# Kernel optimization log

Measured on AMD Instinct MI355X. Metric: run time of the kernel, lower is better.

The kernel has to match this reference:

```python
import jax, jax.numpy as jnp
import numpy as np

N = 100000   # nodes in batched graph
E = 1600000  # edges (before self-loops)
D = 128      # in_dim == hidden_dim == num_outputs
G = 64       # graphs in the batch


def setup_inputs() -> dict:
    key = jax.random.key(0)
    ks = jax.random.split(key, 8)
    s = 1.0 / np.sqrt(D)
    x = jax.random.normal(ks[0], (N, D), jnp.float32)
    src = jax.random.randint(ks[1], (E,), 0, N, dtype=jnp.int64)
    dst = jax.random.randint(ks[2], (E,), 0, N, dtype=jnp.int64)
    graph_ids = jnp.sort(jax.random.randint(ks[3], (N,), 0, G, dtype=jnp.int64))
    W0 = jax.random.normal(ks[4], (D, D), jnp.float32) * s
    W1 = jax.random.normal(ks[5], (D, D), jnp.float32) * s
    W2 = jax.random.normal(ks[6], (D, D), jnp.float32) * s
    b0 = jnp.zeros((D,), jnp.float32)
    b1 = jnp.zeros((D,), jnp.float32)
    b2 = jnp.zeros((D,), jnp.float32)
    return {"x": x, "W0": W0, "b0": b0, "W1": W1, "b1": b1,
            "W2": W2, "b2": b2, "src": src, "dst": dst, "graph_ids": graph_ids}


def reference(x, W0, b0, W1, b1, W2, b2, src, dst, graph_ids):
    n = x.shape[0]
    loops = jnp.arange(n, dtype=src.dtype)
    src_f = jnp.concatenate([src, loops])  # add self-loops once (dgl.add_self_loop)
    dst_f = jnp.concatenate([dst, loops])
    ones_e = jnp.ones(src_f.shape, x.dtype)
    deg_out = jax.ops.segment_sum(ones_e, src_f, num_segments=n)  # >=1 (self-loop)
    deg_in = jax.ops.segment_sum(ones_e, dst_f, num_segments=n)
    cs = jax.lax.rsqrt(deg_out)[:, None]  # source norm (GraphConv norm='both')
    cd = jax.lax.rsqrt(deg_in)[:, None]   # destination norm

    def gcn_layer(h, W, b):
        m = (h * cs)[src_f]                                   # [E+N, D] gather
        agg = jax.ops.segment_sum(m, dst_f, num_segments=n)   # scatter-add SpMM
        return jax.nn.relu((agg * cd) @ W + b)                # F.relu(conv(g, h))

    h = gcn_layer(x, W0, b0)
    h = gcn_layer(h, W1, b1)
    h = gcn_layer(h, W2, b2)

    # dgl.mean_nodes: per-graph mean over nodes
    sums = jax.ops.segment_sum(h, graph_ids, num_segments=G)
    cnt = jax.ops.segment_sum(jnp.ones((n, 1), h.dtype), graph_ids, num_segments=G)
    return sums / jnp.maximum(cnt, 1.0)  # [G, D] logits
```

## Files before the change

### kernel.cpp

```cpp
#include <hip/hip_runtime.h>
#include <stdint.h>

#define D 128
#define CAP 64
#define HB 128
#define CH 50000

typedef __attribute__((ext_vector_type(8))) short bf16x8;
typedef __attribute__((ext_vector_type(4))) float f32x4;
typedef __attribute__((ext_vector_type(2))) float f32x2;

__device__ inline unsigned short f2bf(float x) {
  union { float f; uint32_t u; } v; v.f = x;
  uint32_t u = v.u;
  u += 0x7fffu + ((u >> 16) & 1u);
  return (unsigned short)(u >> 16);
}
__device__ inline uint32_t packbf(float lo, float hi) {
  return (uint32_t)f2bf(lo) | ((uint32_t)f2bf(hi) << 16);
}
__device__ inline f32x2 fp8x2f(uint32_t u) {
  f32x2 r;
  asm("v_cvt_pk_f32_fp8 %0, %1" : "=v"(r) : "v"(u));
  return r;
}
__device__ inline uint32_t f2fp8x2(float a, float b) {
  uint32_t p = 0;
  asm("v_cvt_pk_fp8_f32 %0, %1, %2" : "+v"(p) : "v"(a), "v"(b));
  return p;
}

__global__ __launch_bounds__(512) void hist_kernel(
    const int* __restrict__ src, const int* __restrict__ dst,
    unsigned int* __restrict__ parts_s, unsigned int* __restrict__ parts_d,
    int E, int N,
    const float* __restrict__ W0, const float* __restrict__ W1,
    const float* __restrict__ W2, unsigned short* __restrict__ Wt,
    int* __restrict__ cnt, int G, float* __restrict__ outz, int out_total) {
  __shared__ unsigned int lbs[CH / 8];
  __shared__ unsigned int lbd[CH / 8];
  int b = blockIdx.x & (HB - 1);
  int lo = (blockIdx.x >> 7) * CH;
  for (int i = threadIdx.x; i < CH / 8; i += 512) { lbs[i] = 0; lbd[i] = 0; }
  __syncthreads();
  int per = (E + HB - 1) / HB;
  int e0 = b * per;
  int e1 = min(e0 + per, E);
  for (int e = e0 + threadIdx.x; e < e1; e += 512) {
    int rs = src[e] - lo;
    if ((unsigned)rs < CH) atomicAdd(&lbs[rs >> 3], 1u << ((rs & 7) * 4));
    int rd = dst[e] - lo;
    if ((unsigned)rd < CH) atomicAdd(&lbd[rd >> 3], 1u << ((rd & 7) * 4));
  }
  __syncthreads();
  int nu = (N + 7) / 8;
  int base = lo >> 3;
  int cu = min(CH / 8, nu - base);
  unsigned int* ps = parts_s + (size_t)b * nu + base;
  unsigned int* pd = parts_d + (size_t)b * nu + base;
  for (int i = threadIdx.x; i < cu; i += 512) { ps[i] = lbs[i]; pd[i] = lbd[i]; }

  int gs = gridDim.x * 512;
  for (int i = blockIdx.x * 512 + threadIdx.x; i < 3 * 16384; i += gs) {
    int l = i >> 14, r = i & 16383;
    int n = r >> 7, k = r & 127;
    const float* W = (l == 0) ? W0 : (l == 1) ? W1 : W2;
    Wt[i] = f2bf(W[k * 128 + n]);
  }
  for (int i = blockIdx.x * 512 + threadIdx.x; i < G; i += gs) cnt[i] = 0;
  for (int i = blockIdx.x * 512 + threadIdx.x; i < out_total; i += gs) outz[i] = 0.f;
}

__global__ __launch_bounds__(256) void scan_norm_kernel(
    const unsigned char* __restrict__ parts_s,
    const unsigned char* __restrict__ parts_d,
    unsigned char* __restrict__ offs_d,
    int* __restrict__ degd,
    float* __restrict__ cs, float* __restrict__ cd,
    const int* __restrict__ gid, int* __restrict__ cnt,
    int N, int G) {
  __shared__ int lcnt[256];
  for (int i = threadIdx.x; i < G; i += 256) lcnt[i] = 0;
  __syncthreads();

  int t = blockIdx.x * 256 + threadIdx.x;
  if (t < N) {
    int nb = N / 2;
    int half = t >> 1;
    int sh = (t & 1) * 4;
    int ds = 0, dd = 0;
    for (int bb = 0; bb < HB; bb += 16) {
      unsigned char svv[16], dvv[16];
#pragma unroll
      for (int k = 0; k < 16; k++) {
        svv[k] = parts_s[(size_t)(bb + k) * nb + half];
        dvv[k] = parts_d[(size_t)(bb + k) * nb + half];
      }
#pragma unroll
      for (int k = 0; k < 16; k++) {
        ds += (svv[k] >> sh) & 15;
        offs_d[(size_t)(bb + k) * N + t] = (unsigned char)min(dd, 255);
        dd += (dvv[k] >> sh) & 15;
      }
    }
    degd[t] = dd;
    cs[t] = rsqrtf((float)ds + 1.0f);
    cd[t] = rsqrtf((float)dd + 1.0f);
    atomicAdd(&lcnt[gid[t]], 1);
  }
  __syncthreads();
  for (int i = threadIdx.x; i < G; i += 256) {
    int c = lcnt[i];
    if (c) atomicAdd(&cnt[i], c);
  }
}

__global__ __launch_bounds__(256) void xs_kernel(
    const float* __restrict__ x, const float* __restrict__ cs,
    uint32_t* __restrict__ xs, int N) {
  int total4 = N * 32;
  int gs = gridDim.x * 256;
  for (int i = blockIdx.x * 256 + threadIdx.x; i < total4; i += gs) {
    float4 v = ((const float4*)x)[i];
    float cc = cs[i >> 5];
    uint32_t plo = f2fp8x2(v.x * cc, v.y * cc);
    uint32_t phi = f2fp8x2(v.z * cc, v.w * cc);
    xs[i] = (plo & 0xffffu) | (phi << 16);
  }
}

__global__ __launch_bounds__(512) void fill_kernel(
    const int* __restrict__ src, const int* __restrict__ dst,
    const unsigned char* __restrict__ offs_d, int* __restrict__ col, int E, int N) {
  __shared__ unsigned int lcur[CH / 8];
  int b = blockIdx.x & (HB - 1);
  int lo = (blockIdx.x >> 7) * CH;
  for (int i = threadIdx.x; i < CH / 8; i += 512) lcur[i] = 0;
  __syncthreads();
  int per = (E + HB - 1) / HB;
  int e0 = b * per;
  int e1 = min(e0 + per, E);
  const unsigned char* offb = offs_d + (size_t)b * N;
  int e = e0 + threadIdx.x;
  for (; e + 1536 < e1; e += 2048) {
    int dd4[4], ss4[4], rd4[4];
    unsigned char ob4[4];
#pragma unroll
    for (int k = 0; k < 4; k++) { dd4[k] = dst[e + k * 512]; ss4[k] = src[e + k * 512]; }
#pragma unroll
    for (int k = 0; k < 4; k++) {
      rd4[k] = dd4[k] - lo;
      ob4[k] = ((unsigned)rd4[k] < CH) ? offb[dd4[k]] : (unsigned char)0;
    }
#pragma unroll
    for (int k = 0; k < 4; k++) {
      if ((unsigned)rd4[k] < CH) {
        unsigned old = atomicAdd(&lcur[rd4[k] >> 3], 1u << ((rd4[k] & 7) * 4));
        int local = (old >> ((rd4[k] & 7) * 4)) & 0xF;
        int pos = (int)ob4[k] + local;
        if (pos < CAP) col[(size_t)dd4[k] * CAP + pos] = ss4[k];
      }
    }
  }
  for (; e < e1; e += 512) {
    int d = dst[e];
    int rd = d - lo;
    if ((unsigned)rd < CH) {
      unsigned old = atomicAdd(&lcur[rd >> 3], 1u << ((rd & 7) * 4));
      int local = (old >> ((rd & 7) * 4)) & 0xF;
      int pos = (int)offb[d] + local;
      if (pos < CAP) col[(size_t)d * CAP + pos] = src[e];
    }
  }
}

__global__ __launch_bounds__(512) void fused_layer_kernel(
    const unsigned short* __restrict__ hin, const unsigned short* __restrict__ Wt,
    const float* __restrict__ bias, const float* __restrict__ cd,
    const float* __restrict__ rowscale, const int* __restrict__ degd,
    const int* __restrict__ col, unsigned short* __restrict__ hout, int N) {
  __shared__ __align__(16) uint32_t At[16 * 68];

  int wv = threadIdx.x >> 6;
  int lane = threadIdx.x & 63;
  int m = lane & 15;
  int quad = lane >> 4;

  bf16x8 bfr[4];
#pragma unroll
  for (int c = 0; c < 4; c++)
    bfr[c] = *(const bf16x8*)(Wt + (size_t)(16 * wv + m) * 128 + c * 32 + quad * 8);

#pragma unroll
  for (int j = 0; j < 2; j++) {
    int w = __builtin_amdgcn_readfirstlane(blockIdx.x * 16 + wv * 2 + j);
    float accx = 0.f, accy = 0.f;
    if (w < N) {
      int n = min(degd[w], CAP);
      const int* cw = col + (size_t)w * CAP;
      const unsigned short* hl = hin + lane;
      f32x2 sf = fp8x2f(hl[(size_t)w * 64]);
      accx = sf.x; accy = sf.y;
      int i = 0;
      for (; i + 7 < n; i += 8) {
        int s0 = cw[i],     s1 = cw[i + 1], s2 = cw[i + 2], s3 = cw[i + 3];
        int s4 = cw[i + 4], s5 = cw[i + 5], s6 = cw[i + 6], s7 = cw[i + 7];
        uint32_t v0 = hl[(size_t)s0 * 64];
        uint32_t v1 = hl[(size_t)s1 * 64];
        uint32_t v2 = hl[(size_t)s2 * 64];
        uint32_t v3 = hl[(size_t)s3 * 64];
        uint32_t v4 = hl[(size_t)s4 * 64];
        uint32_t v5 = hl[(size_t)s5 * 64];
        uint32_t v6 = hl[(size_t)s6 * 64];
        uint32_t v7 = hl[(size_t)s7 * 64];
        f32x2 f0 = fp8x2f(v0), f1 = fp8x2f(v1), f2 = fp8x2f(v2), f3 = fp8x2f(v3);
        f32x2 f4 = fp8x2f(v4), f5 = fp8x2f(v5), f6 = fp8x2f(v6), f7 = fp8x2f(v7);
        accx += f0.x; accy += f0.y;
        accx += f1.x; accy += f1.y;
        accx += f2.x; accy += f2.y;
        accx += f3.x; accy += f3.y;
        accx += f4.x; accy += f4.y;
        accx += f5.x; accy += f5.y;
        accx += f6.x; accy += f6.y;
        accx += f7.x; accy += f7.y;
      }
      for (; i + 3 < n; i += 4) {
        int s0 = cw[i], s1 = cw[i + 1], s2 = cw[i + 2], s3 = cw[i + 3];
        uint32_t v0 = hl[(size_t)s0 * 64];
        uint32_t v1 = hl[(size_t)s1 * 64];
        uint32_t v2 = hl[(size_t)s2 * 64];
        uint32_t v3 = hl[(size_t)s3 * 64];
        f32x2 f0 = fp8x2f(v0), f1 = fp8x2f(v1), f2 = fp8x2f(v2), f3 = fp8x2f(v3);
        accx += f0.x; accy += f0.y;
        accx += f1.x; accy += f1.y;
        accx += f2.x; accy += f2.y;
        accx += f3.x; accy += f3.y;
      }
      for (; i < n; i++) {
        f32x2 f = fp8x2f(hl[(size_t)cw[i] * 64]);
        accx += f.x; accy += f.y;
      }
      float cdv = cd[w];
      accx *= cdv; accy *= cdv;
    }
    At[(wv * 2 + j) * 68 + lane] = packbf(accx, accy);
  }
  __syncthreads();

  const unsigned short* arow = (const unsigned short*)At + m * 136;
  f32x4 acc = f32x4{0.f, 0.f, 0.f, 0.f};
#pragma unroll
  for (int c = 0; c < 4; c++) {
    bf16x8 a = *(const bf16x8*)(arow + c * 32 + quad * 8);
    acc = __builtin_amdgcn_mfma_f32_16x16x32_bf16(a, bfr[c], acc, 0, 0, 0);
  }
  int colb = 16 * wv + m;
  float bv = bias[colb];
  if (rowscale) {
    unsigned char* h8 = (unsigned char*)hout;
#pragma unroll
    for (int i = 0; i < 4; i++) {
      int r = blockIdx.x * 16 + quad * 4 + i;
      if (r < N) {
        float v = acc[i] + bv;
        v = v > 0.f ? v : 0.f;
        v *= rowscale[r];
        h8[(size_t)r * D + colb] = (unsigned char)(f2fp8x2(v, v) & 0xffu);
      }
    }
  } else {
#pragma unroll
    for (int i = 0; i < 4; i++) {
      int r = blockIdx.x * 16 + quad * 4 + i;
      if (r < N) {
        float v = acc[i] + bv;
        v = v > 0.f ? v : 0.f;
        hout[(size_t)r * D + colb] = f2bf(v);
      }
    }
  }
}

__global__ void pool_kernel(const unsigned short* __restrict__ h, const int* __restrict__ gid,
                            float* __restrict__ outsum, const int* __restrict__ cnt, int N) {
  int v0 = blockIdx.x * 64;
  if (v0 >= N) return;
  int d = threadIdx.x;
  int vend = min(v0 + 64, N);
  int cur = gid[v0];
  float acc = 0.f;
  for (int v = v0; v < vend; v++) {
    int g = gid[v];
    if (g != cur) {
      float inv = 1.0f / fmaxf((float)cnt[cur], 1.0f);
      atomicAdd(&outsum[cur * D + d], acc * inv);
      acc = 0.f; cur = g;
    }
    unsigned short hv = __builtin_nontemporal_load(&h[(size_t)v * D + d]);
    union { uint32_t u; float f; } cv; cv.u = (uint32_t)hv << 16;
    acc += cv.f;
  }
  float inv = 1.0f / fmaxf((float)cnt[cur], 1.0f);
  atomicAdd(&outsum[cur * D + d], acc * inv);
}

extern "C" void kernel_launch(void* const* d_in, const int* in_sizes, int n_in,
                              void* d_out, int out_size, void* d_ws, size_t ws_size,
                              hipStream_t stream) {
  const float* x  = (const float*)d_in[0];
  const float* W0 = (const float*)d_in[1];
  const float* b0 = (const float*)d_in[2];
  const float* W1 = (const float*)d_in[3];
  const float* b1 = (const float*)d_in[4];
  const float* W2 = (const float*)d_in[5];
  const float* b2 = (const float*)d_in[6];
  const int* src  = (const int*)d_in[7];
  const int* dst  = (const int*)d_in[8];
  const int* gid  = (const int*)d_in[9];

  const int N = in_sizes[0] / D;
  const int E = in_sizes[7];
  const int G = out_size / D;
  const int nu = (N + 7) / 8;

  uint32_t* hsA = (uint32_t*)d_ws;
  uint32_t* hsB = hsA + (size_t)N * 64;
  int* col      = (int*)(hsB + (size_t)N * 64);
  int* degd     = col + (size_t)N * CAP;
  float* csb    = (float*)(degd + N);
  float* cdb    = csb + N;
  int* cnt      = (int*)(cdb + N);
  unsigned short* Wt = (unsigned short*)(cnt + G);
  unsigned int* parts_s = (unsigned int*)(Wt + 3 * 16384);
  unsigned int* parts_d = parts_s + (size_t)HB * nu;
  unsigned char* offs_d = (unsigned char*)(parts_d + (size_t)HB * nu);

  const int nch = (N + CH - 1) / CH;
  hist_kernel<<<HB * nch, 512, 0, stream>>>(src, dst, parts_s, parts_d, E, N,
                                            W0, W1, W2, Wt, cnt, G,
                                            (float*)d_out, out_size);
  scan_norm_kernel<<<(N + 255) / 256, 256, 0, stream>>>(
      (const unsigned char*)parts_s, (const unsigned char*)parts_d, offs_d,
      degd, csb, cdb, gid, cnt, N, G);
  xs_kernel<<<1024, 256, 0, stream>>>(x, csb, hsA, N);
  fill_kernel<<<HB * nch, 512, 0, stream>>>(src, dst, offs_d, col, E, N);

  const int ltiles = (N + 15) / 16;

  fused_layer_kernel<<<ltiles, 512, 0, stream>>>((const unsigned short*)hsA, Wt, b0,
                                                 cdb, csb, degd, col,
                                                 (unsigned short*)hsB, N);
  fused_layer_kernel<<<ltiles, 512, 0, stream>>>((const unsigned short*)hsB, Wt + 16384, b1,
                                                 cdb, csb, degd, col,
                                                 (unsigned short*)hsA, N);
  fused_layer_kernel<<<ltiles, 512, 0, stream>>>((const unsigned short*)hsA, Wt + 2 * 16384, b2,
                                                 cdb, nullptr, degd, col,
                                                 (unsigned short*)hsB, N);

  pool_kernel<<<(N + 63) / 64, 128, 0, stream>>>((const unsigned short*)hsB, gid,
                                                 (float*)d_out, cnt, N);
}
```

Measured before the change: 376.9 us.

## Replace histogram/scan CSR build with chunk-bucketed routing and global atomics

Replaces the 4-bit packed shared-memory histogram, per-block prefix scan and fill kernels with a two-pass bucket sort. The first pass routes edges into 8192-node chunk buckets, and the second pass scatters them into the column array using global atomic degree counters, with chunks spread across XCD-interleaved blocks. This removes the large per-partition offset tables and the repeated full passes over the edge list, so the new path streams edges once. In exchange, slot order inside each node's column list becomes nondeterministic, the code relies on global atomics and fixed bucket capacities, and it adds memset launches.

```diff
diff --git a/kernel.cpp b/kernel.cpp
--- a/kernel.cpp
+++ b/kernel.cpp
@@ -3,8 +3,10 @@
 
 #define D 128
 #define CAP 64
-#define HB 128
-#define CH 50000
+#define NCHK 16
+#define CSH 13
+#define CNODES 8192
+#define BCAP 262144
 
 typedef __attribute__((ext_vector_type(8))) short bf16x8;
 typedef __attribute__((ext_vector_type(4))) float f32x4;
@@ -30,82 +32,106 @@
   return p;
 }
 
-__global__ __launch_bounds__(512) void hist_kernel(
+__global__ __launch_bounds__(256) void route_kernel(
     const int* __restrict__ src, const int* __restrict__ dst,
-    unsigned int* __restrict__ parts_s, unsigned int* __restrict__ parts_d,
-    int E, int N,
+    uint32_t* __restrict__ bucketD, unsigned short* __restrict__ bucketS,
+    int* __restrict__ gcurD, int* __restrict__ gcurS, int E,
     const float* __restrict__ W0, const float* __restrict__ W1,
-    const float* __restrict__ W2, unsigned short* __restrict__ Wt,
-    int* __restrict__ cnt, int G, float* __restrict__ outz, int out_total) {
-  __shared__ unsigned int lbs[CH / 8];
-  __shared__ unsigned int lbd[CH / 8];
-  int b = blockIdx.x & (HB - 1);
-  int lo = (blockIdx.x >> 7) * CH;
-  for (int i = threadIdx.x; i < CH / 8; i += 512) { lbs[i] = 0; lbd[i] = 0; }
-  __syncthreads();
-  int per = (E + HB - 1) / HB;
-  int e0 = b * per;
-  int e1 = min(e0 + per, E);
-  for (int e = e0 + threadIdx.x; e < e1; e += 512) {
-    int rs = src[e] - lo;
-    if ((unsigned)rs < CH) atomicAdd(&lbs[rs >> 3], 1u << ((rs & 7) * 4));
-    int rd = dst[e] - lo;
-    if ((unsigned)rd < CH) atomicAdd(&lbd[rd >> 3], 1u << ((rd & 7) * 4));
-  }
-  __syncthreads();
-  int nu = (N + 7) / 8;
-  int base = lo >> 3;
-  int cu = min(CH / 8, nu - base);
-  unsigned int* ps = parts_s + (size_t)b * nu + base;
-  unsigned int* pd = parts_d + (size_t)b * nu + base;
-  for (int i = threadIdx.x; i < cu; i += 512) { ps[i] = lbs[i]; pd[i] = lbd[i]; }
-
-  int gs = gridDim.x * 512;
-  for (int i = blockIdx.x * 512 + threadIdx.x; i < 3 * 16384; i += gs) {
+    const float* __restrict__ W2, unsigned short* __restrict__ Wt) {
+  __shared__ int cntD[NCHK], cntS[NCHK], baseD[NCHK], baseS[NCHK];
+  int ntiles = (E + 2047) / 2048;
+  for (int tile = blockIdx.x; tile < ntiles; tile += gridDim.x) {
+    int e0 = tile * 2048;
+    int s[8], d[8];
+#pragma unroll
+    for (int k = 0; k < 8; k++) {
+      int e = e0 + k * 256 + threadIdx.x;
+      if (e < E) { s[k] = src[e]; d[k] = dst[e]; } else { s[k] = -1; d[k] = -1; }
+    }
+    if (threadIdx.x < NCHK) { cntD[threadIdx.x] = 0; cntS[threadIdx.x] = 0; }
+    __syncthreads();
+#pragma unroll
+    for (int k = 0; k < 8; k++)
+      if (d[k] >= 0) {
+        atomicAdd(&cntD[d[k] >> CSH], 1);
+        atomicAdd(&cntS[s[k] >> CSH], 1);
+      }
+    __syncthreads();
+    if (threadIdx.x < NCHK) {
+      baseD[threadIdx.x] = atomicAdd(&gcurD[threadIdx.x], cntD[threadIdx.x]);
+      baseS[threadIdx.x] = atomicAdd(&gcurS[threadIdx.x], cntS[threadIdx.x]);
+      cntD[threadIdx.x] = 0; cntS[threadIdx.x] = 0;
+    }
+    __syncthreads();
+#pragma unroll
+    for (int k = 0; k < 8; k++)
+      if (d[k] >= 0) {
+        int cD = d[k] >> CSH;
+        int slot = atomicAdd(&cntD[cD], 1);
+        bucketD[(size_t)cD * BCAP + baseD[cD] + slot] =
+            ((uint32_t)(d[k] & (CNODES - 1)) << 17) | (uint32_t)s[k];
+        int cS = s[k] >> CSH;
+        int slot2 = atomicAdd(&cntS[cS], 1);
+        bucketS[(size_t)cS * BCAP + baseS[cS] + slot2] =
+            (unsigned short)(s[k] & (CNODES - 1));
+      }
+    __syncthreads();
+  }
+  int gs = gridDim.x * 256;
+  for (int i = blockIdx.x * 256 + threadIdx.x; i < 3 * 16384; i += gs) {
     int l = i >> 14, r = i & 16383;
     int n = r >> 7, k = r & 127;
     const float* W = (l == 0) ? W0 : (l == 1) ? W1 : W2;
     Wt[i] = f2bf(W[k * 128 + n]);
   }
-  for (int i = blockIdx.x * 512 + threadIdx.x; i < G; i += gs) cnt[i] = 0;
-  for (int i = blockIdx.x * 512 + threadIdx.x; i < out_total; i += gs) outz[i] = 0.f;
-}
-
-__global__ __launch_bounds__(256) void scan_norm_kernel(
-    const unsigned char* __restrict__ parts_s,
-    const unsigned char* __restrict__ parts_d,
-    unsigned char* __restrict__ offs_d,
-    int* __restrict__ degd,
+}
+
+__global__ __launch_bounds__(256) void scatter_kernel(
+    const uint32_t* __restrict__ bucketD, const unsigned short* __restrict__ bucketS,
+    const int* __restrict__ gcurD, const int* __restrict__ gcurS,
+    int* __restrict__ col, int* __restrict__ degd, int* __restrict__ degs,
+    int nchk) {
+  int xcd = blockIdx.x & 7;
+  int slot = blockIdx.x >> 3;
+  int two = (xcd + 8 < nchk) ? 1 : 0;
+  int c, sub, nsub;
+  if (two) {
+    if (slot < 16) { c = xcd; sub = slot; nsub = 16; }
+    else           { c = xcd + 8; sub = slot - 16; nsub = 16; }
+  } else { c = xcd; sub = slot; nsub = 32; }
+  if (c >= nchk) return;
+  int base = c * CNODES;
+  int nE = gcurD[c];
+  int lo = (int)((long long)nE * sub / nsub);
+  int hi = (int)((long long)nE * (sub + 1) / nsub);
+  const uint32_t* bd = bucketD + (size_t)c * BCAP;
+  for (int i = lo + threadIdx.x; i < hi; i += 256) {
+    uint32_t p = bd[i];
+    int dg = base + (int)(p >> 17);
+    int s = (int)(p & 0x1FFFFu);
+    int pos = atomicAdd(&degd[dg], 1);
+    if (pos < CAP) col[(size_t)dg * CAP + pos] = s;
+  }
+  int nS = gcurS[c];
+  lo = (int)((long long)nS * sub / nsub);
+  hi = (int)((long long)nS * (sub + 1) / nsub);
+  const unsigned short* bs = bucketS + (size_t)c * BCAP;
+  for (int i = lo + threadIdx.x; i < hi; i += 256) {
+    atomicAdd(&degs[base + bs[i]], 1);
+  }
+}
+
+__global__ __launch_bounds__(256) void norm_kernel(
+    const int* __restrict__ degs, const int* __restrict__ degd,
     float* __restrict__ cs, float* __restrict__ cd,
-    const int* __restrict__ gid, int* __restrict__ cnt,
-    int N, int G) {
+    const int* __restrict__ gid, int* __restrict__ cnt, int N, int G) {
   __shared__ int lcnt[256];
   for (int i = threadIdx.x; i < G; i += 256) lcnt[i] = 0;
   __syncthreads();
-
   int t = blockIdx.x * 256 + threadIdx.x;
   if (t < N) {
-    int nb = N / 2;
-    int half = t >> 1;
-    int sh = (t & 1) * 4;
-    int ds = 0, dd = 0;
-    for (int bb = 0; bb < HB; bb += 16) {
-      unsigned char svv[16], dvv[16];
-#pragma unroll
-      for (int k = 0; k < 16; k++) {
-        svv[k] = parts_s[(size_t)(bb + k) * nb + half];
-        dvv[k] = parts_d[(size_t)(bb + k) * nb + half];
-      }
-#pragma unroll
-      for (int k = 0; k < 16; k++) {
-        ds += (svv[k] >> sh) & 15;
-        offs_d[(size_t)(bb + k) * N + t] = (unsigned char)min(dd, 255);
-        dd += (dvv[k] >> sh) & 15;
-      }
-    }
-    degd[t] = dd;
-    cs[t] = rsqrtf((float)ds + 1.0f);
-    cd[t] = rsqrtf((float)dd + 1.0f);
+    cs[t] = rsqrtf((float)degs[t] + 1.0f);
+    cd[t] = rsqrtf((float)degd[t] + 1.0f);
     atomicAdd(&lcnt[gid[t]], 1);
   }
   __syncthreads();
@@ -126,51 +152,6 @@
     uint32_t plo = f2fp8x2(v.x * cc, v.y * cc);
     uint32_t phi = f2fp8x2(v.z * cc, v.w * cc);
     xs[i] = (plo & 0xffffu) | (phi << 16);
-  }
-}
-
-__global__ __launch_bounds__(512) void fill_kernel(
-    const int* __restrict__ src, const int* __restrict__ dst,
-    const unsigned char* __restrict__ offs_d, int* __restrict__ col, int E, int N) {
-  __shared__ unsigned int lcur[CH / 8];
-  int b = blockIdx.x & (HB - 1);
-  int lo = (blockIdx.x >> 7) * CH;
-  for (int i = threadIdx.x; i < CH / 8; i += 512) lcur[i] = 0;
-  __syncthreads();
-  int per = (E + HB - 1) / HB;
-  int e0 = b * per;
-  int e1 = min(e0 + per, E);
-  const unsigned char* offb = offs_d + (size_t)b * N;
-  int e = e0 + threadIdx.x;
-  for (; e + 1536 < e1; e += 2048) {
-    int dd4[4], ss4[4], rd4[4];
-    unsigned char ob4[4];
-#pragma unroll
-    for (int k = 0; k < 4; k++) { dd4[k] = dst[e + k * 512]; ss4[k] = src[e + k * 512]; }
-#pragma unroll
-    for (int k = 0; k < 4; k++) {
-      rd4[k] = dd4[k] - lo;
-      ob4[k] = ((unsigned)rd4[k] < CH) ? offb[dd4[k]] : (unsigned char)0;
-    }
-#pragma unroll
-    for (int k = 0; k < 4; k++) {
-      if ((unsigned)rd4[k] < CH) {
-        unsigned old = atomicAdd(&lcur[rd4[k] >> 3], 1u << ((rd4[k] & 7) * 4));
-        int local = (old >> ((rd4[k] & 7) * 4)) & 0xF;
-        int pos = (int)ob4[k] + local;
-        if (pos < CAP) col[(size_t)dd4[k] * CAP + pos] = ss4[k];
-      }
-    }
-  }
-  for (; e < e1; e += 512) {
-    int d = dst[e];
-    int rd = d - lo;
-    if ((unsigned)rd < CH) {
-      unsigned old = atomicAdd(&lcur[rd >> 3], 1u << ((rd & 7) * 4));
-      int local = (old >> ((rd & 7) * 4)) & 0xF;
-      int pos = (int)offb[d] + local;
-      if (pos < CAP) col[(size_t)d * CAP + pos] = src[e];
-    }
   }
 }
 
@@ -321,29 +302,33 @@
   const int N = in_sizes[0] / D;
   const int E = in_sizes[7];
   const int G = out_size / D;
-  const int nu = (N + 7) / 8;
 
   uint32_t* hsA = (uint32_t*)d_ws;
   uint32_t* hsB = hsA + (size_t)N * 64;
   int* col      = (int*)(hsB + (size_t)N * 64);
   int* degd     = col + (size_t)N * CAP;
-  float* csb    = (float*)(degd + N);
+  int* degs     = degd + N;
+  int* cnt      = degs + N;
+  int* gcurD    = cnt + G;
+  int* gcurS    = gcurD + NCHK;
+  float* csb    = (float*)(gcurS + NCHK);
   float* cdb    = csb + N;
-  int* cnt      = (int*)(cdb + N);
-  unsigned short* Wt = (unsigned short*)(cnt + G);
-  unsigned int* parts_s = (unsigned int*)(Wt + 3 * 16384);
-  unsigned int* parts_d = parts_s + (size_t)HB * nu;
-  unsigned char* offs_d = (unsigned char*)(parts_d + (size_t)HB * nu);
-
-  const int nch = (N + CH - 1) / CH;
-  hist_kernel<<<HB * nch, 512, 0, stream>>>(src, dst, parts_s, parts_d, E, N,
-                                            W0, W1, W2, Wt, cnt, G,
-                                            (float*)d_out, out_size);
-  scan_norm_kernel<<<(N + 255) / 256, 256, 0, stream>>>(
-      (const unsigned char*)parts_s, (const unsigned char*)parts_d, offs_d,
-      degd, csb, cdb, gid, cnt, N, G);
+  unsigned short* Wt = (unsigned short*)(cdb + N);
+  uint32_t* bucketD  = (uint32_t*)(Wt + 3 * 16384);
+  unsigned short* bucketS = (unsigned short*)(bucketD + (size_t)NCHK * BCAP);
+
+  const int nchk = (N + CNODES - 1) >> CSH;
+
+  hipMemsetAsync(degd, 0, (size_t)(2 * N + G + 2 * NCHK) * sizeof(int), stream);
+  hipMemsetAsync(d_out, 0, (size_t)out_size * sizeof(float), stream);
+
+  route_kernel<<<512, 256, 0, stream>>>(src, dst, bucketD, bucketS,
+                                        gcurD, gcurS, E, W0, W1, W2, Wt);
+  scatter_kernel<<<256, 256, 0, stream>>>(bucketD, bucketS, gcurD, gcurS,
+                                          col, degd, degs, nchk);
+  norm_kernel<<<(N + 255) / 256, 256, 0, stream>>>(degs, degd, csb, cdb,
+                                                   gid, cnt, N, G);
   xs_kernel<<<1024, 256, 0, stream>>>(x, csb, hsA, N);
-  fill_kernel<<<HB * nch, 512, 0, stream>>>(src, dst, offs_d, col, E, N);
 
   const int ltiles = (N + 15) / 16;
 
```

Result: slower. 477.8 us (+26.8%).
